# Kernel tuning notes

Hardware: AMD Instinct MI355X
Metric: run time of the kernel (lower is better)

## Reference

```python
import jax, jax.numpy as jnp
import numpy as np

N_NODES = 50000
N_EDGES = 600000
N_LABEL = 200000
IN_CH = 128
OUT_CH = 128
K_HOPS = 2


def setup_inputs() -> dict:
    key = jax.random.key(0)
    ks = jax.random.split(key, 9)
    x = jax.random.normal(ks[0], (N_NODES, IN_CH), dtype=jnp.float32)
    edge_index = jax.random.randint(ks[1], (2, N_EDGES), 0, N_NODES)
    edge_label_index = jax.random.randint(ks[2], (2, N_LABEL), 0, N_NODES)
    conv_weight = jax.random.normal(ks[3], (OUT_CH, IN_CH), dtype=jnp.float32) * 0.05
    conv_bias = jax.random.normal(ks[4], (OUT_CH,), dtype=jnp.float32) * 0.05
    w1 = jax.random.normal(ks[5], (OUT_CH // 2, OUT_CH), dtype=jnp.float32) * 0.05
    b1 = jax.random.normal(ks[6], (OUT_CH // 2,), dtype=jnp.float32) * 0.05
    w2 = jax.random.normal(ks[7], (1, OUT_CH // 2), dtype=jnp.float32) * 0.05
    b2 = jax.random.normal(ks[8], (1,), dtype=jnp.float32) * 0.05
    return {"x": x, "edge_index": edge_index, "edge_label_index": edge_label_index,
            "conv_weight": conv_weight, "conv_bias": conv_bias,
            "w1": w1, "b1": b1, "w2": w2, "b2": b2}


def reference(x, edge_index, edge_label_index, conv_weight, conv_bias, w1, b1, w2, b2):
    n = x.shape[0]
    # gcn_norm with self-loops: A_hat = D^{-1/2} (A + I) D^{-1/2}
    loop = jnp.arange(n, dtype=edge_index.dtype)
    src = jnp.concatenate([edge_index[0], loop])  # message sources
    dst = jnp.concatenate([edge_index[1], loop])  # aggregation targets
    deg = jax.ops.segment_sum(jnp.ones_like(dst, dtype=x.dtype), dst, num_segments=n)
    dinv = jnp.where(deg > 0, jax.lax.rsqrt(deg), 0.0)
    w = dinv[src] * dinv[dst]  # [E+N] edge weights

    # K-hop propagation: h <- A_hat h, repeated K times (SGConv)
    h = x
    for _ in range(K_HOPS):
        h = jax.ops.segment_sum(h[src] * w[:, None], dst, num_segments=n)
    z = h @ conv_weight.T + conv_bias  # [N, out_channels]

    # decode: gather endpoint embeddings, multiply, tiny MLP (dropout inactive at eval)
    s = z[edge_label_index[0]] * z[edge_label_index[1]]  # [E_label, out]
    h1 = jax.nn.relu(s @ w1.T + b1)
    r = (h1 @ w2.T + b2).sum(axis=-1)  # [E_label]
    return r
```

## Files before the change

kernel.cpp:

```cpp
#include <hip/hip_runtime.h>

#define N_CH 128
#define SLOT 64

typedef _Float16 half8  __attribute__((ext_vector_type(8)));
typedef _Float16 half4v __attribute__((ext_vector_type(4)));
typedef float    floatx4 __attribute__((ext_vector_type(4)));
typedef unsigned int uint4v __attribute__((ext_vector_type(4)));


__global__ void k_prep(int* __restrict__ cur,
                       const float* __restrict__ W,  _Float16* __restrict__ wh,
                       const float* __restrict__ W1, _Float16* __restrict__ w1h,
                       int n) {
    int i = blockIdx.x * blockDim.x + threadIdx.x;
    if (i < n) cur[i] = 0;
    int nw4  = N_CH * N_CH / 4;
    int nw14 = 64 * N_CH / 4;
    if (i < nw4) {
        float4 v = ((const float4*)W)[i];
        half4v o;
        o[0] = (_Float16)v.x; o[1] = (_Float16)v.y; o[2] = (_Float16)v.z; o[3] = (_Float16)v.w;
        ((half4v*)wh)[i] = o;
    } else if (i < nw4 + nw14) {
        int j = i - nw4;
        float4 v = ((const float4*)W1)[j];
        half4v o;
        o[0] = (_Float16)v.x; o[1] = (_Float16)v.y; o[2] = (_Float16)v.z; o[3] = (_Float16)v.w;
        ((half4v*)w1h)[j] = o;
    }
}


__global__ void k_fillfix(const int* __restrict__ src, const int* __restrict__ dst,
                          int* __restrict__ cur, unsigned short* __restrict__ csr, int E) {
    int e = blockIdx.x * blockDim.x + threadIdx.x;
    if (e < E) {
        int d = dst[e];
        int p = atomicAdd(&cur[d], 1);
        if (p < SLOT) csr[d * SLOT + p] = (unsigned short)src[e];
    }
}


__global__ __launch_bounds__(256) void k_metascale(
        const int* __restrict__ cur, int2* __restrict__ meta,
        unsigned short* __restrict__ csr,
        const float* __restrict__ x,
        _Float16* __restrict__ u0, _Float16* __restrict__ u1, int n) {
    int i = blockIdx.x * blockDim.x + threadIdx.x;
    int tot = n * 16;
    if (i < tot) {
        int node = i >> 4, chunk = i & 15;
        int ct = cur[node];
        float d = rsqrtf((float)(ct + 1));
        int c = (ct < SLOT) ? ct : SLOT;
        if (chunk == 0) {
            int cp = (c + 7) & ~7;
            unsigned short zn = (unsigned short)n;
            for (int j = c; j < cp; ++j) csr[node * SLOT + j] = zn;
            int2 mv; mv.x = cp >> 3; mv.y = __float_as_int(d);
            meta[node] = mv;
        }
        float4 v0 = ((const float4*)x)[node * 32 + chunk * 2];
        float4 v1 = ((const float4*)x)[node * 32 + chunk * 2 + 1];
        half8 o;
        o[0] = (_Float16)(d * v0.x); o[1] = (_Float16)(d * v0.y);
        o[2] = (_Float16)(d * v0.z); o[3] = (_Float16)(d * v0.w);
        o[4] = (_Float16)(d * v1.x); o[5] = (_Float16)(d * v1.y);
        o[6] = (_Float16)(d * v1.z); o[7] = (_Float16)(d * v1.w);
        ((half8*)u0)[node * 16 + chunk] = o;
    } else if (i < tot + 32) {
        int j = i - tot;
        _Float16* d16 = (j < 16) ? u0 : u1;
        half8 zz;
        #pragma unroll
        for (int q = 0; q < 8; ++q) zz[q] = (_Float16)0.f;
        ((half8*)d16)[n * 16 + (j & 15)] = zz;
    }
}


__global__ __launch_bounds__(256) void k_hop16(const _Float16* __restrict__ hin,
                                               _Float16* __restrict__ hout,
                                               const int2* __restrict__ meta,
                                               const unsigned short* __restrict__ csr,
                                               int n) {
    int tid = threadIdx.x;
    int node = blockIdx.x * 16 + (tid >> 4);
    if (node >= n) return;
    int c = tid & 15;
    int2 mv = meta[node];
    int nq = mv.x;
    float di = __int_as_float(mv.y);
    float sc = di * di;
    const uint4v* qlst = (const uint4v*)(csr + node * SLOT);
    const half8* hp = (const half8*)hin;
    half8 self = hp[node * 16 + c];
    float acc[8];
    #pragma unroll
    for (int j = 0; j < 8; ++j) acc[j] = (float)self[j];
    uint4v pk = qlst[0];
    #pragma unroll 1
    for (int q = 0; q < nq; ++q) {
        uint4v nx = qlst[q + 1];
        int idx[8];
        idx[0] = pk[0] & 0xFFFF; idx[1] = pk[0] >> 16;
        idx[2] = pk[1] & 0xFFFF; idx[3] = pk[1] >> 16;
        idx[4] = pk[2] & 0xFFFF; idx[5] = pk[2] >> 16;
        idx[6] = pk[3] & 0xFFFF; idx[7] = pk[3] >> 16;
        half8 u[8];
        #pragma unroll
        for (int i = 0; i < 8; ++i)
            u[i] = hp[idx[i] * 16 + c];
        #pragma unroll
        for (int i = 0; i < 8; ++i)
            #pragma unroll
            for (int j = 0; j < 8; ++j) acc[j] += (float)u[i][j];
        pk = nx;
    }
    half8 o;
    #pragma unroll
    for (int j = 0; j < 8; ++j) o[j] = (_Float16)(sc * acc[j]);
    ((half8*)hout)[node * 16 + c] = o;
}


__global__ __launch_bounds__(512, 4) void k_hopz(const _Float16* __restrict__ hin,
                                                 const int2* __restrict__ meta,
                                                 const unsigned short* __restrict__ csr,
                                                 const _Float16* __restrict__ wh,
                                                 const float* __restrict__ bc,
                                                 _Float16* __restrict__ z, int n) {
    __shared__ half8 wls[128 * 16];
    __shared__ half8 sls[128 * 16];
    int tid = threadIdx.x;
    int lane = tid & 63, w = tid >> 6;
    int quad = lane >> 4, m16 = lane & 15;
    int nb = blockIdx.x * 128;
    #pragma unroll
    for (int i = 0; i < 4; ++i) {
        int g = tid + 512 * i;
        int r = g >> 4, cc = g & 15;
        wls[r * 16 + (cc ^ (r & 15))] = ((const half8*)wh)[g];
    }
    int grp = tid >> 4;
    int c = tid & 15;
    const half8* hp = (const half8*)hin;
    #pragma unroll 1
    for (int s = 0; s < 4; ++s) {
        int r = grp + 32 * s;
        int node = nb + r;
        half8 o;
        if (node < n) {
            int2 mv = meta[node];
            int nq = mv.x;
            float di = __int_as_float(mv.y);
            const uint4v* qlst = (const uint4v*)(csr + node * SLOT);
            half8 self = hp[node * 16 + c];
            float acc[8];
            #pragma unroll
            for (int j = 0; j < 8; ++j) acc[j] = (float)self[j];
            uint4v pk = qlst[0];
            #pragma unroll 1
            for (int q = 0; q < nq; ++q) {
                uint4v nx = qlst[q + 1];
                int idx[8];
                idx[0] = pk[0] & 0xFFFF; idx[1] = pk[0] >> 16;
                idx[2] = pk[1] & 0xFFFF; idx[3] = pk[1] >> 16;
                idx[4] = pk[2] & 0xFFFF; idx[5] = pk[2] >> 16;
                idx[6] = pk[3] & 0xFFFF; idx[7] = pk[3] >> 16;
                half8 u[8];
                #pragma unroll
                for (int i = 0; i < 8; ++i)
                    u[i] = hp[idx[i] * 16 + c];
                #pragma unroll
                for (int i = 0; i < 8; ++i)
                    #pragma unroll
                    for (int j = 0; j < 8; ++j) acc[j] += (float)u[i][j];
                pk = nx;
            }
            #pragma unroll
            for (int j = 0; j < 8; ++j) o[j] = (_Float16)(di * acc[j]);
        } else {
            #pragma unroll
            for (int j = 0; j < 8; ++j) o[j] = (_Float16)0.f;
        }
        sls[r * 16 + (c ^ (r & 15))] = o;
    }
    __syncthreads();
    half8 a[4];
    #pragma unroll
    for (int kk = 0; kk < 4; ++kk)
        a[kk] = sls[(w * 16 + m16) * 16 + ((kk * 4 + quad) ^ m16)];
    int outnode0 = nb + w * 16 + quad * 4;
    #pragma unroll
    for (int jt = 0; jt < 8; ++jt) {
        floatx4 acc = {0.f, 0.f, 0.f, 0.f};
        #pragma unroll
        for (int kk = 0; kk < 4; ++kk) {
            int r = jt * 16 + m16;
            half8 bfr = wls[r * 16 + ((kk * 4 + quad) ^ m16)];
            acc = __builtin_amdgcn_mfma_f32_16x16x32_f16(a[kk], bfr, acc, 0, 0, 0);
        }
        int j = jt * 16 + m16;
        float bias = bc[j];
        #pragma unroll
        for (int reg = 0; reg < 4; ++reg) {
            int node = outnode0 + reg;
            if (node < n) z[(size_t)node * N_CH + j] = (_Float16)(acc[reg] + bias);
        }
    }
}


__global__ __launch_bounds__(256) void k_decode_mfma(const _Float16* __restrict__ z,
        const int* __restrict__ ai, const int* __restrict__ bi,
        const _Float16* __restrict__ w1h, const float* __restrict__ b1,
        const float* __restrict__ w2, const float* __restrict__ b2,
        float* __restrict__ out, int m) {
    __shared__ half8 w1ls[64 * 16];
    __shared__ half8 sls[64 * 16];
    int tid = threadIdx.x;
    int lane = tid & 63, w = tid >> 6;
    int quad = lane >> 4, m16 = lane & 15;
    int pbase = blockIdx.x * 64;
    #pragma unroll
    for (int i = 0; i < 4; ++i) {
        int g = tid + 256 * i;
        int r = g >> 4, c = g & 15;
        w1ls[r * 16 + (c ^ (r & 15))] = ((const half8*)w1h)[g];
    }
    int pidx = pbase + w * 16 + m16;
    if (pidx >= m) pidx = m - 1;
    int idxa = ai[pidx];
    int idxb = bi[pidx];
    int ia[4], ib[4];
    #pragma unroll
    for (int it = 0; it < 4; ++it) {
        int p = it * 4 + quad;
        ia[it] = __shfl(idxa, p, 64);
        ib[it] = __shfl(idxb, p, 64);
    }
    half8 za[4], zb[4];
    #pragma unroll
    for (int it = 0; it < 4; ++it) {
        za[it] = ((const half8*)(z + (size_t)ia[it] * N_CH))[m16];
        zb[it] = ((const half8*)(z + (size_t)ib[it] * N_CH))[m16];
    }
    #pragma unroll
    for (int it = 0; it < 4; ++it) {
        half8 s8 = za[it] * zb[it];
        int pp = w * 16 + it * 4 + quad;
        sls[pp * 16 + (m16 ^ (pp & 15))] = s8;
    }
    __syncthreads();
    half8 a[4];
    #pragma unroll
    for (int kk = 0; kk < 4; ++kk)
        a[kk] = sls[(w * 16 + m16) * 16 + ((kk * 4 + quad) ^ m16)];
    float rsum[4] = {0.f, 0.f, 0.f, 0.f};
    #pragma unroll
    for (int jt = 0; jt < 4; ++jt) {
        floatx4 acc = {0.f, 0.f, 0.f, 0.f};
        #pragma unroll
        for (int kk = 0; kk < 4; ++kk) {
            int r = jt * 16 + m16;
            half8 bfr = w1ls[r * 16 + ((kk * 4 + quad) ^ m16)];
            acc = __builtin_amdgcn_mfma_f32_16x16x32_f16(a[kk], bfr, acc, 0, 0, 0);
        }
        int j = jt * 16 + m16;
        float b1j = b1[j], w2j = w2[j];
        #pragma unroll
        for (int reg = 0; reg < 4; ++reg) {
            float v = fmaxf(acc[reg] + b1j, 0.f) * w2j;
            v += __shfl_xor(v, 1, 64);
            v += __shfl_xor(v, 2, 64);
            v += __shfl_xor(v, 4, 64);
            v += __shfl_xor(v, 8, 64);
            rsum[reg] += v;
        }
    }
    if (m16 == 0) {
        float bb = b2[0];
        #pragma unroll
        for (int reg = 0; reg < 4; ++reg) {
            int gp = pbase + w * 16 + quad * 4 + reg;
            if (gp < m) out[gp] = rsum[reg] + bb;
        }
    }
}


extern "C" void kernel_launch(void* const* d_in, const int* in_sizes, int n_in,
                              void* d_out, int out_size, void* d_ws, size_t ws_size,
                              hipStream_t stream) {
    const float* x   = (const float*)d_in[0];
    const int*   ei  = (const int*)d_in[1];
    const int*   eli = (const int*)d_in[2];
    const float* W   = (const float*)d_in[3];
    const float* bc  = (const float*)d_in[4];
    const float* W1  = (const float*)d_in[5];
    const float* b1  = (const float*)d_in[6];
    const float* w2  = (const float*)d_in[7];
    const float* b2  = (const float*)d_in[8];
    float* out = (float*)d_out;

    const int N = in_sizes[0] / N_CH;
    const int E = in_sizes[1] / 2;
    const int M = in_sizes[2] / 2;

    const int* src = ei;
    const int* dst = ei + E;
    const int* ai  = eli;
    const int* bi  = eli + M;

    _Float16* hb0 = (_Float16*)d_ws;
    _Float16* hb1 = hb0 + (size_t)(N + 1) * N_CH;
    _Float16* wh  = hb1 + (size_t)(N + 1) * N_CH;
    _Float16* w1h = wh + 16384;
    unsigned short* csr = (unsigned short*)(w1h + 8192);
    int2*  meta = (int2*)(csr + (size_t)N * SLOT + 64);
    int*   cur  = (int*)(meta + N);

    k_prep<<<(N + 255) / 256, 256, 0, stream>>>(cur, W, wh, W1, w1h, N);
    k_fillfix<<<(E + 255) / 256, 256, 0, stream>>>(src, dst, cur, csr, E);
    int mw = N * 16 + 32;
    k_metascale<<<(mw + 255) / 256, 256, 0, stream>>>(cur, meta, csr, x, hb0, hb1, N);

    int nblk = (N + 15) / 16;
    k_hop16<<<nblk, 256, 0, stream>>>(hb0, hb1, meta, csr, N);
    k_hopz<<<(N + 127) / 128, 512, 0, stream>>>(hb1, meta, csr, wh, bc, hb0, N);

    k_decode_mfma<<<(M + 63) / 64, 256, 0, stream>>>(hb0, ai, bi, w1h, b1, w2, b2, out, M);
}
```

Baseline: 192.0 us.

## Bucket nodes by padded degree to balance gather work across wavefronts

Adds two kernels that histogram nodes by their 8-neighbour chunk count and then write a permutation, ordered by that count, that also carries packed node id and normalisation. Both hop kernels now process nodes in this order, so threads in a wavefront loop a similar number of times, which reduces divergence and tail imbalance. In exchange there are two extra launches with atomics, an indirect node lookup, scattered output writes, and worse locality of the self-row reads.

```diff
diff --git a/kernel.cpp b/kernel.cpp
--- a/kernel.cpp
+++ b/kernel.cpp
@@ -9,12 +9,13 @@
 typedef unsigned int uint4v __attribute__((ext_vector_type(4)));
 
 
-__global__ void k_prep(int* __restrict__ cur,
+__global__ void k_prep(int* __restrict__ cur, int* __restrict__ bins,
                        const float* __restrict__ W,  _Float16* __restrict__ wh,
                        const float* __restrict__ W1, _Float16* __restrict__ w1h,
                        int n) {
     int i = blockIdx.x * blockDim.x + threadIdx.x;
     if (i < n) cur[i] = 0;
+    if (i < 32) bins[i] = 0;
     int nw4  = N_CH * N_CH / 4;
     int nw14 = 64 * N_CH / 4;
     if (i < nw4) {
@@ -43,8 +44,65 @@
 }
 
 
+__global__ __launch_bounds__(256) void k_bcount(const int* __restrict__ cur,
+                                                int* __restrict__ bcnt, int n) {
+    int i = blockIdx.x * 256 + threadIdx.x;
+    int b = -1;
+    if (i < n) {
+        int ct = cur[i];
+        int c = (ct < SLOT) ? ct : SLOT;
+        b = ((c + 7) & ~7) >> 3;
+    }
+    int lane = threadIdx.x & 63;
+    #pragma unroll
+    for (int k = 0; k <= 8; ++k) {
+        unsigned long long m = __ballot(b == k);
+        if (m != 0ull && lane == (__ffsll(m) - 1))
+            atomicAdd(&bcnt[k], __popcll(m));
+    }
+}
+
+
+__global__ __launch_bounds__(256) void k_order(const int* __restrict__ cur,
+                                               const int* __restrict__ bcnt,
+                                               int* __restrict__ bcur,
+                                               int2* __restrict__ morder,
+                                               int n, int ntot) {
+    int i = blockIdx.x * 256 + threadIdx.x;
+    int b = -1, np8 = 0;
+    float d = 0.f;
+    if (i < n) {
+        int ct = cur[i];
+        int c = (ct < SLOT) ? ct : SLOT;
+        np8 = ((c + 7) & ~7) >> 3;
+        b = np8;
+        d = rsqrtf((float)(ct + 1));
+    } else if (i < ntot) {
+        int2 s; s.x = n; s.y = 0;
+        morder[i] = s;
+    }
+    int lane = threadIdx.x & 63;
+    #pragma unroll
+    for (int k = 0; k <= 8; ++k) {
+        unsigned long long m = __ballot(b == k);
+        if (m == 0ull) continue;
+        int leader = __ffsll(m) - 1;
+        int pb = 0;
+        if (lane == leader) pb = atomicAdd(&bcur[k], __popcll(m));
+        pb = __shfl(pb, leader, 64);
+        if (b == k) {
+            int base = 0;
+            for (int t = 0; t < k; ++t) base += bcnt[t];
+            int rank = __popcll(m & ((1ull << lane) - 1ull));
+            int2 mv; mv.x = i | (np8 << 20); mv.y = __float_as_int(d);
+            morder[base + pb + rank] = mv;
+        }
+    }
+}
+
+
 __global__ __launch_bounds__(256) void k_metascale(
-        const int* __restrict__ cur, int2* __restrict__ meta,
+        const int* __restrict__ cur,
         unsigned short* __restrict__ csr,
         const float* __restrict__ x,
         _Float16* __restrict__ u0, _Float16* __restrict__ u1, int n) {
@@ -59,8 +117,6 @@
             int cp = (c + 7) & ~7;
             unsigned short zn = (unsigned short)n;
             for (int j = c; j < cp; ++j) csr[node * SLOT + j] = zn;
-            int2 mv; mv.x = cp >> 3; mv.y = __float_as_int(d);
-            meta[node] = mv;
         }
         float4 v0 = ((const float4*)x)[node * 32 + chunk * 2];
         float4 v1 = ((const float4*)x)[node * 32 + chunk * 2 + 1];
@@ -83,15 +139,15 @@
 
 __global__ __launch_bounds__(256) void k_hop16(const _Float16* __restrict__ hin,
                                                _Float16* __restrict__ hout,
-                                               const int2* __restrict__ meta,
+                                               const int2* __restrict__ morder,
                                                const unsigned short* __restrict__ csr,
                                                int n) {
     int tid = threadIdx.x;
-    int node = blockIdx.x * 16 + (tid >> 4);
-    if (node >= n) return;
+    int pos = blockIdx.x * 16 + (tid >> 4);
     int c = tid & 15;
-    int2 mv = meta[node];
-    int nq = mv.x;
+    int2 mv = morder[pos];
+    int node = mv.x & 0xFFFFF;
+    int nq = mv.x >> 20;
     float di = __int_as_float(mv.y);
     float sc = di * di;
     const uint4v* qlst = (const uint4v*)(csr + node * SLOT);
@@ -127,7 +183,7 @@
 
 
 __global__ __launch_bounds__(512, 4) void k_hopz(const _Float16* __restrict__ hin,
-                                                 const int2* __restrict__ meta,
+                                                 const int2* __restrict__ morder,
                                                  const unsigned short* __restrict__ csr,
                                                  const _Float16* __restrict__ wh,
                                                  const float* __restrict__ bc,
@@ -150,42 +206,37 @@
     #pragma unroll 1
     for (int s = 0; s < 4; ++s) {
         int r = grp + 32 * s;
-        int node = nb + r;
+        int2 mv = morder[nb + r];
+        int node = mv.x & 0xFFFFF;
+        int nq = mv.x >> 20;
+        float di = __int_as_float(mv.y);
+        const uint4v* qlst = (const uint4v*)(csr + node * SLOT);
+        half8 self = hp[node * 16 + c];
+        float acc[8];
+        #pragma unroll
+        for (int j = 0; j < 8; ++j) acc[j] = (float)self[j];
+        uint4v pk = qlst[0];
+        #pragma unroll 1
+        for (int q = 0; q < nq; ++q) {
+            uint4v nx = qlst[q + 1];
+            int idx[8];
+            idx[0] = pk[0] & 0xFFFF; idx[1] = pk[0] >> 16;
+            idx[2] = pk[1] & 0xFFFF; idx[3] = pk[1] >> 16;
+            idx[4] = pk[2] & 0xFFFF; idx[5] = pk[2] >> 16;
+            idx[6] = pk[3] & 0xFFFF; idx[7] = pk[3] >> 16;
+            half8 u[8];
+            #pragma unroll
+            for (int i = 0; i < 8; ++i)
+                u[i] = hp[idx[i] * 16 + c];
+            #pragma unroll
+            for (int i = 0; i < 8; ++i)
+                #pragma unroll
+                for (int j = 0; j < 8; ++j) acc[j] += (float)u[i][j];
+            pk = nx;
+        }
         half8 o;
-        if (node < n) {
-            int2 mv = meta[node];
-            int nq = mv.x;
-            float di = __int_as_float(mv.y);
-            const uint4v* qlst = (const uint4v*)(csr + node * SLOT);
-            half8 self = hp[node * 16 + c];
-            float acc[8];
-            #pragma unroll
-            for (int j = 0; j < 8; ++j) acc[j] = (float)self[j];
-            uint4v pk = qlst[0];
-            #pragma unroll 1
-            for (int q = 0; q < nq; ++q) {
-                uint4v nx = qlst[q + 1];
-                int idx[8];
-                idx[0] = pk[0] & 0xFFFF; idx[1] = pk[0] >> 16;
-                idx[2] = pk[1] & 0xFFFF; idx[3] = pk[1] >> 16;
-                idx[4] = pk[2] & 0xFFFF; idx[5] = pk[2] >> 16;
-                idx[6] = pk[3] & 0xFFFF; idx[7] = pk[3] >> 16;
-                half8 u[8];
-                #pragma unroll
-                for (int i = 0; i < 8; ++i)
-                    u[i] = hp[idx[i] * 16 + c];
-                #pragma unroll
-                for (int i = 0; i < 8; ++i)
-                    #pragma unroll
-                    for (int j = 0; j < 8; ++j) acc[j] += (float)u[i][j];
-                pk = nx;
-            }
-            #pragma unroll
-            for (int j = 0; j < 8; ++j) o[j] = (_Float16)(di * acc[j]);
-        } else {
-            #pragma unroll
-            for (int j = 0; j < 8; ++j) o[j] = (_Float16)0.f;
-        }
+        #pragma unroll
+        for (int j = 0; j < 8; ++j) o[j] = (_Float16)(di * acc[j]);
         sls[r * 16 + (c ^ (r & 15))] = o;
     }
     __syncthreads();
@@ -193,7 +244,11 @@
     #pragma unroll
     for (int kk = 0; kk < 4; ++kk)
         a[kk] = sls[(w * 16 + m16) * 16 + ((kk * 4 + quad) ^ m16)];
-    int outnode0 = nb + w * 16 + quad * 4;
+    int outpos0 = nb + w * 16 + quad * 4;
+    int nodeo[4];
+    #pragma unroll
+    for (int reg = 0; reg < 4; ++reg)
+        nodeo[reg] = ((const int*)morder)[2 * (outpos0 + reg)] & 0xFFFFF;
     #pragma unroll
     for (int jt = 0; jt < 8; ++jt) {
         floatx4 acc = {0.f, 0.f, 0.f, 0.f};
@@ -207,8 +262,8 @@
         float bias = bc[j];
         #pragma unroll
         for (int reg = 0; reg < 4; ++reg) {
-            int node = outnode0 + reg;
-            if (node < n) z[(size_t)node * N_CH + j] = (_Float16)(acc[reg] + bias);
+            if (nodeo[reg] < n)
+                z[(size_t)nodeo[reg] * N_CH + j] = (_Float16)(acc[reg] + bias);
         }
     }
 }
@@ -309,6 +364,7 @@
     const int N = in_sizes[0] / N_CH;
     const int E = in_sizes[1] / 2;
     const int M = in_sizes[2] / 2;
+    const int NTOT = (N + 127) & ~127;
 
     const int* src = ei;
     const int* dst = ei + E;
@@ -320,17 +376,19 @@
     _Float16* wh  = hb1 + (size_t)(N + 1) * N_CH;
     _Float16* w1h = wh + 16384;
     unsigned short* csr = (unsigned short*)(w1h + 8192);
-    int2*  meta = (int2*)(csr + (size_t)N * SLOT + 64);
-    int*   cur  = (int*)(meta + N);
-
-    k_prep<<<(N + 255) / 256, 256, 0, stream>>>(cur, W, wh, W1, w1h, N);
+    int2*  morder = (int2*)(csr + (size_t)N * SLOT + 64);
+    int*   cur  = (int*)(morder + NTOT);
+    int*   bins = cur + N;
+
+    k_prep<<<(N + 255) / 256, 256, 0, stream>>>(cur, bins, W, wh, W1, w1h, N);
     k_fillfix<<<(E + 255) / 256, 256, 0, stream>>>(src, dst, cur, csr, E);
+    k_bcount<<<(N + 255) / 256, 256, 0, stream>>>(cur, bins, N);
+    k_order<<<(NTOT + 255) / 256, 256, 0, stream>>>(cur, bins, bins + 16, morder, N, NTOT);
     int mw = N * 16 + 32;
-    k_metascale<<<(mw + 255) / 256, 256, 0, stream>>>(cur, meta, csr, x, hb0, hb1, N);
-
-    int nblk = (N + 15) / 16;
-    k_hop16<<<nblk, 256, 0, stream>>>(hb0, hb1, meta, csr, N);
-    k_hopz<<<(N + 127) / 128, 512, 0, stream>>>(hb1, meta, csr, wh, bc, hb0, N);
+    k_metascale<<<(mw + 255) / 256, 256, 0, stream>>>(cur, csr, x, hb0, hb1, N);
+
+    k_hop16<<<NTOT / 16, 256, 0, stream>>>(hb0, hb1, morder, csr, N);
+    k_hopz<<<NTOT / 128, 512, 0, stream>>>(hb1, morder, csr, wh, bc, hb0, N);
 
     k_decode_mfma<<<(M + 63) / 64, 256, 0, stream>>>(hb0, ai, bi, w1h, b1, w2, b2, out, M);
 }
```

Result: slower. 251.4 us (+31.0%).
